# Performance work log

Measured on AMD Instinct MI355X. Metric: run time of the kernel, lower is better.

The kernel has to match this reference:

```python
import jax, jax.numpy as jnp
import numpy as np

B, T, V, F = 32, 128, 128, 64
K_ORDER = 3
N_FILT = 64

def setup_inputs() -> dict:
    key = jax.random.key(0)
    k1, k2, k3 = jax.random.split(key, 3)
    x = jax.random.normal(k1, (B, T, V, F), dtype=jnp.float32)
    W = jax.random.uniform(k2, (B, V, V), dtype=jnp.float32)  # learned adjacency, nonneg
    # keras 'uniform' initializer default range [-0.05, 0.05]
    Theta = jax.random.uniform(k3, (K_ORDER, F, N_FILT), dtype=jnp.float32, minval=-0.05, maxval=0.05)
    return {"x": x, "W": W, "Theta": Theta}

def reference(x, W, Theta):
    # x: (B,T,V,F), W: (B,V,V), Theta: (k,F,O)
    k = Theta.shape[0]
    v = x.shape[2]
    eye = jnp.eye(v, dtype=x.dtype)
    deg = jnp.sum(W, axis=1)                      # (B,V) -- sum over axis=1 as in K.sum(W, axis=1)
    D = eye[None, :, :] * deg[:, :, None]         # matrix_diag(deg)
    L = D - W
    L_t = L - eye[None, :, :]                     # 2*L/lambda_max - I with lambda_max=2
    chebs = [jnp.broadcast_to(eye[None, :, :], W.shape), L_t]
    for i in range(2, k):
        # NOTE: elementwise multiply, faithful to the original tf code (tf `*`)
        chebs.append(2.0 * L_t * chebs[-1] - chebs[-2])
    Tk = jnp.stack(chebs, axis=0)                 # (k,B,V,V)
    # out[b,t,u,o] = sum_{k,v,f} Tk[k,b,v,u] * x[b,t,v,f] * Theta[k,f,o]
    # (T_k transposed matmul graph_signal, then dot with theta_k, summed over k and t-batched)
    out = jnp.einsum('kbvu,btvf,kfo->btuo', Tk, x, Theta)
    return jax.nn.relu(out)
```

## Files before the change

### kernel.cpp

```cpp
#include <hip/hip_runtime.h>

typedef __attribute__((ext_vector_type(8))) short bf16x8;
typedef __attribute__((ext_vector_type(4))) float f32x4;

namespace {

constexpr int B = 32, T = 128, V = 128, F = 64, O = 64;
constexpr int TPB = 8;

constexpr size_t WS_THT_OFF = (size_t)B * 64 * 64 * 8 * 2;
constexpr size_t WS_LDG_OFF = WS_THT_OFF + 1536 * 8 * 2;

__device__ inline unsigned short f2bf(float f) {
    unsigned u = __builtin_bit_cast(unsigned, f);
    u += 0x7FFFu + ((u >> 16) & 1u);
    return (unsigned short)(u >> 16);
}

__global__ __launch_bounds__(256) void prep(const float* __restrict__ W,
                                            const float* __restrict__ Theta,
                                            unsigned short* __restrict__ acat_f,
                                            unsigned short* __restrict__ tht_f,
                                            float* __restrict__ ldg) {
    const int tid = threadIdx.x;
    if (blockIdx.x == B) {
        for (int i = 0; i < 6; ++i) {
            int fi = tid + i * 256;
            int ks = fi / 768, rem = fi % 768;
            int nf = rem >> 6, lane = rem & 63;
            int n = nf * 16 + (lane & 15);
            int f0 = ks * 32 + (lane >> 4) * 8;
            unsigned short vals[8];
#pragma unroll
            for (int j = 0; j < 8; ++j) {
                int f = f0 + j;
                float v;
                if (n < 64)       v = Theta[f * 64 + n] - Theta[2 * 4096 + f * 64 + n];
                else if (n < 128) v = Theta[4096 + f * 64 + (n - 64)];
                else              v = Theta[2 * 4096 + f * 64 + (n - 128)];
                vals[j] = f2bf(v);
            }
            *(bf16x8*)(tht_f + (size_t)fi * 8) = *(bf16x8*)vals;
        }
        return;
    }
    const int b = blockIdx.x;
    const float* Wb = W + (size_t)b * V * V;
    __shared__ float Wl[V][V + 1];
    for (int i = 0; i < V * V / 256; ++i) {
        int idx = tid + i * 256;
        Wl[idx >> 7][idx & 127] = Wb[idx];
    }
    __syncthreads();
    if (tid < V) {
        float s = 0.f;
        for (int i = 0; i < V; ++i) s += Wl[i][tid];
        ldg[b * V + tid] = s - 1.0f - Wl[tid][tid];
    }
    unsigned short* ab_f = acat_f + (size_t)b * 32768;
    for (int i = 0; i < 16; ++i) {
        int fi = tid + i * 256;
        int ks = fi >> 9, rem = fi & 511;
        int r2 = rem >> 6, lane = rem & 63;
        int u = r2 * 16 + (lane & 15);
        int kv0 = ks * 32 + (lane >> 4) * 8;
        unsigned short vals[8];
#pragma unroll
        for (int j = 0; j < 8; ++j) {
            int kv = kv0 + j, v = kv & 127;
            float wv = Wl[v][u];
            float val = (v == u) ? 0.f : ((kv < 128) ? -wv : 2.f * wv * wv);
            vals[j] = f2bf(val);
        }
        *(bf16x8*)(ab_f + (size_t)fi * 8) = *(bf16x8*)vals;
    }
}

__global__ __launch_bounds__(512, 4) void graph_conv_main(
    const float* __restrict__ x, const unsigned short* __restrict__ acat_f,
    const unsigned short* __restrict__ tht_f, const float* __restrict__ ldg,
    float* __restrict__ out) {
    const int t0 = blockIdx.x * TPB, b = blockIdx.y;
    const int tid = threadIdx.x;
    const int lane = tid & 63, w = tid >> 6;
    const int lr = lane & 15, lg = lane >> 4;

    __shared__ __align__(16) unsigned short tht_s[12288];
    __shared__ __align__(16) unsigned short xbuf[2][8192];
    __shared__ __align__(16) unsigned short zc1[4096];
    __shared__ __align__(16) unsigned short zc2[4096];

    const float* xb = x + ((size_t)(b * T + t0)) * (V * F);

#pragma unroll
    for (int i = 0; i < 3; ++i) {
        int c = tid + i * 512;
        __builtin_amdgcn_global_load_lds(
            (const __attribute__((address_space(1))) void*)(tht_f + c * 8),
            (__attribute__((address_space(3))) void*)(tht_s + c * 8), 16, 0, 0);
    }

    bf16x8 af_r[8];
#pragma unroll
    for (int ks = 0; ks < 8; ++ks)
        af_r[ks] = *(const bf16x8*)(acat_f + (((size_t)b * 64 + ks * 8 + w) * 64 + lane) * 8);

    const float* ldb = ldg + b * V;
    const f32x4 ldv = *(const f32x4*)(ldb + 16 * w + lg * 4);
    const f32x4 ld2v = 2.0f * ldv * ldv;

    float4 pf[4];
    auto load_pf = [&](int tt) {
        const float4* src = (const float4*)(xb + (size_t)tt * (V * F));
#pragma unroll
        for (int i = 0; i < 4; ++i) pf[i] = src[tid + i * 512];
    };
    auto store_pf = [&](int buf) {
#pragma unroll
        for (int i = 0; i < 4; ++i) {
            int p = tid + i * 512;
            int row = p >> 4, c4 = p & 15;
            uint2 q;
            q.x = f2bf(pf[i].x) | ((unsigned)f2bf(pf[i].y) << 16);
            q.y = f2bf(pf[i].z) | ((unsigned)f2bf(pf[i].w) << 16);
            *(uint2*)((char*)xbuf[buf] + row * 128 + ((c4 * 8) ^ ((row & 7) << 4))) = q;
        }
    };

    load_pf(0);
    store_pf(0);
    __syncthreads();
    int cur = 0;

    for (int tt = 0; tt < TPB; ++tt) {
        if (tt + 1 < TPB) load_pf(tt + 1);

        bf16x8 xa[2];
        {
            const int row = 16 * w + lr;
            const int rb = row * 128, rs = (row & 7) << 4;
#pragma unroll
            for (int ks = 0; ks < 2; ++ks)
                xa[ks] = *(const bf16x8*)((const char*)xbuf[cur] + rb + ((ks * 64 + lg * 16) ^ rs));
        }

        f32x4 acc[4], z[4];
#pragma unroll
        for (int of = 0; of < 4; ++of) {
            acc[of] = (f32x4){0.f, 0.f, 0.f, 0.f};
            z[of] = (f32x4){0.f, 0.f, 0.f, 0.f};
        }

#pragma unroll
        for (int ks = 0; ks < 2; ++ks)
#pragma unroll
            for (int nf = 0; nf < 8; ++nf) {
                bf16x8 tb = *(const bf16x8*)(tht_s + ((ks * 12 + nf) * 64 + lane) * 8);
                if (nf < 4) acc[nf] = __builtin_amdgcn_mfma_f32_16x16x32_bf16(xa[ks], tb, acc[nf], 0, 0, 0);
                else        z[nf - 4] = __builtin_amdgcn_mfma_f32_16x16x32_bf16(xa[ks], tb, z[nf - 4], 0, 0, 0);
            }

        {
            const int vcol = 16 * w + lg * 4;
#pragma unroll
            for (int of = 0; of < 4; ++of) {
                acc[of] += ldv * z[of];
                const int rowz = of * 16 + lr;
                f32x4 zv = z[of];
                uint2 q;
                q.x = f2bf(zv[0]) | ((unsigned)f2bf(zv[1]) << 16);
                q.y = f2bf(zv[2]) | ((unsigned)f2bf(zv[3]) << 16);
                *(uint2*)((char*)zc1 + rowz * 256 + ((vcol * 2) ^ ((rowz & 7) << 4))) = q;
                z[of] = (f32x4){0.f, 0.f, 0.f, 0.f};
            }
        }

#pragma unroll
        for (int ks = 0; ks < 2; ++ks)
#pragma unroll
            for (int nf = 0; nf < 4; ++nf) {
                bf16x8 tb = *(const bf16x8*)(tht_s + ((ks * 12 + 8 + nf) * 64 + lane) * 8);
                z[nf] = __builtin_amdgcn_mfma_f32_16x16x32_bf16(xa[ks], tb, z[nf], 0, 0, 0);
            }

        {
            const int vcol = 16 * w + lg * 4;
#pragma unroll
            for (int of = 0; of < 4; ++of) {
                acc[of] += ld2v * z[of];
                const int rowz = of * 16 + lr;
                f32x4 zv = z[of];
                uint2 q;
                q.x = f2bf(zv[0]) | ((unsigned)f2bf(zv[1]) << 16);
                q.y = f2bf(zv[2]) | ((unsigned)f2bf(zv[3]) << 16);
                *(uint2*)((char*)zc2 + rowz * 256 + ((vcol * 2) ^ ((rowz & 7) << 4))) = q;
            }
        }

        __syncthreads();

#pragma unroll
        for (int ks = 0; ks < 8; ++ks) {
            const char* zsrc = (ks < 4) ? (const char*)zc1 : (const char*)zc2;
            const int kcol = (ks & 3) * 64 + lg * 16;
#pragma unroll
            for (int of = 0; of < 4; ++of) {
                const int rowz = of * 16 + lr;
                bf16x8 zb = *(const bf16x8*)(zsrc + rowz * 256 + (kcol ^ ((rowz & 7) << 4)));
                acc[of] = __builtin_amdgcn_mfma_f32_16x16x32_bf16(af_r[ks], zb, acc[of], 0, 0, 0);
            }
        }

        if (tt + 1 < TPB) store_pf(cur ^ 1);

        float* obt = out + ((size_t)(b * T + t0 + tt)) * (V * O);
#pragma unroll
        for (int of = 0; of < 4; ++of)
#pragma unroll
            for (int j = 0; j < 4; ++j) {
                const int u = 16 * w + lg * 4 + j;
                const int o = of * 16 + lr;
                const float r = acc[of][j];
                obt[u * 64 + o] = r > 0.f ? r : 0.f;
            }

        __syncthreads();
        cur ^= 1;
    }
}

}

extern "C" void kernel_launch(void* const* d_in, const int* in_sizes, int n_in,
                              void* d_out, int out_size, void* d_ws, size_t ws_size,
                              hipStream_t stream) {
    const float* x = (const float*)d_in[0];
    const float* W = (const float*)d_in[1];
    const float* Theta = (const float*)d_in[2];
    float* outp = (float*)d_out;

    unsigned short* acat_f = (unsigned short*)d_ws;
    unsigned short* tht_f = (unsigned short*)((char*)d_ws + WS_THT_OFF);
    float* ldg = (float*)((char*)d_ws + WS_LDG_OFF);

    prep<<<B + 1, 256, 0, stream>>>(W, Theta, acat_f, tht_f, ldg);
    graph_conv_main<<<dim3(T / TPB, B), 512, 0, stream>>>(x, acat_f, tht_f, ldg, outp);
}
```

Baseline: 85.19 us.

## Stage x via async global-to-LDS loads in fp32 and double time steps per block

```diff
diff --git a/kernel.cpp b/kernel.cpp
--- a/kernel.cpp
+++ b/kernel.cpp
@@ -6,7 +6,7 @@
 namespace {
 
 constexpr int B = 32, T = 128, V = 128, F = 64, O = 64;
-constexpr int TPB = 8;
+constexpr int TPB = 16;
 
 constexpr size_t WS_THT_OFF = (size_t)B * 64 * 64 * 8 * 2;
 constexpr size_t WS_LDG_OFF = WS_THT_OFF + 1536 * 8 * 2;
@@ -76,7 +76,7 @@
     }
 }
 
-__global__ __launch_bounds__(512, 4) void graph_conv_main(
+__global__ __launch_bounds__(512, 2) void graph_conv_main(
     const float* __restrict__ x, const unsigned short* __restrict__ acat_f,
     const unsigned short* __restrict__ tht_f, const float* __restrict__ ldg,
     float* __restrict__ out) {
@@ -86,11 +86,37 @@
     const int lr = lane & 15, lg = lane >> 4;
 
     __shared__ __align__(16) unsigned short tht_s[12288];
-    __shared__ __align__(16) unsigned short xbuf[2][8192];
-    __shared__ __align__(16) unsigned short zc1[4096];
-    __shared__ __align__(16) unsigned short zc2[4096];
+    __shared__ __align__(16) float xbuf[2][V * F];
+    __shared__ __align__(16) unsigned short zc1[8192];
+    __shared__ __align__(16) unsigned short zc2[8192];
 
     const float* xb = x + ((size_t)(b * T + t0)) * (V * F);
+
+    bf16x8 af_r[8];
+#pragma unroll
+    for (int ks = 0; ks < 8; ++ks)
+        af_r[ks] = *(const bf16x8*)(acat_f + (((size_t)b * 64 + ks * 8 + w) * 64 + lane) * 8);
+    const f32x4 ldv = *(const f32x4*)(ldg + b * V + 16 * w + lg * 4);
+    const f32x4 ld2v = 2.0f * ldv * ldv;
+    asm volatile("s_waitcnt vmcnt(0)" ::: "memory");
+    __builtin_amdgcn_sched_barrier(0);
+
+    auto stage_x = [&](int tt, int buf) {
+        const char* src = (const char*)(xb + (size_t)tt * (V * F));
+        char* lbase = (char*)&xbuf[buf][0] + w * 4096;
+#pragma unroll
+        for (int j = 0; j < 4; ++j) {
+            int a = j * 1024 + lane * 16;
+            int rloc = a >> 8;
+            int slot = (a >> 5) & 7;
+            int within = a & 31;
+            int row = 16 * w + rloc;
+            const char* g = src + row * 256 + ((slot ^ (row & 7)) << 5) + within;
+            __builtin_amdgcn_global_load_lds(
+                (const __attribute__((address_space(1))) void*)g,
+                (__attribute__((address_space(3))) void*)(lbase + j * 1024), 16, 0, 0);
+        }
+    };
 
 #pragma unroll
     for (int i = 0; i < 3; ++i) {
@@ -99,49 +125,35 @@
             (const __attribute__((address_space(1))) void*)(tht_f + c * 8),
             (__attribute__((address_space(3))) void*)(tht_s + c * 8), 16, 0, 0);
     }
-
-    bf16x8 af_r[8];
-#pragma unroll
-    for (int ks = 0; ks < 8; ++ks)
-        af_r[ks] = *(const bf16x8*)(acat_f + (((size_t)b * 64 + ks * 8 + w) * 64 + lane) * 8);
-
-    const float* ldb = ldg + b * V;
-    const f32x4 ldv = *(const f32x4*)(ldb + 16 * w + lg * 4);
-    const f32x4 ld2v = 2.0f * ldv * ldv;
-
-    float4 pf[4];
-    auto load_pf = [&](int tt) {
-        const float4* src = (const float4*)(xb + (size_t)tt * (V * F));
-#pragma unroll
-        for (int i = 0; i < 4; ++i) pf[i] = src[tid + i * 512];
-    };
-    auto store_pf = [&](int buf) {
-#pragma unroll
-        for (int i = 0; i < 4; ++i) {
-            int p = tid + i * 512;
-            int row = p >> 4, c4 = p & 15;
-            uint2 q;
-            q.x = f2bf(pf[i].x) | ((unsigned)f2bf(pf[i].y) << 16);
-            q.y = f2bf(pf[i].z) | ((unsigned)f2bf(pf[i].w) << 16);
-            *(uint2*)((char*)xbuf[buf] + row * 128 + ((c4 * 8) ^ ((row & 7) << 4))) = q;
-        }
-    };
-
-    load_pf(0);
-    store_pf(0);
-    __syncthreads();
+    stage_x(0, 0);
+    asm volatile("s_waitcnt vmcnt(0)" ::: "memory");
+    __builtin_amdgcn_sched_barrier(0);
+    __builtin_amdgcn_s_barrier();
+    __builtin_amdgcn_sched_barrier(0);
+
     int cur = 0;
-
     for (int tt = 0; tt < TPB; ++tt) {
-        if (tt + 1 < TPB) load_pf(tt + 1);
+        if (tt + 1 < TPB) stage_x(tt + 1, cur ^ 1);
+        asm volatile("s_waitcnt vmcnt(4)" ::: "memory");
+        __builtin_amdgcn_sched_barrier(0);
 
         bf16x8 xa[2];
         {
             const int row = 16 * w + lr;
-            const int rb = row * 128, rs = (row & 7) << 4;
-#pragma unroll
-            for (int ks = 0; ks < 2; ++ks)
-                xa[ks] = *(const bf16x8*)((const char*)xbuf[cur] + rb + ((ks * 64 + lg * 16) ^ rs));
+            const char* rbp = (const char*)&xbuf[cur][0] + row * 256;
+            const int rs = row & 7;
+#pragma unroll
+            for (int ks = 0; ks < 2; ++ks) {
+                const char* pa = rbp + (((ks * 4 + lg) ^ rs) << 5);
+                f32x4 a0 = *(const f32x4*)pa;
+                f32x4 a1 = *(const f32x4*)(pa + 16);
+                uint4 u;
+                u.x = f2bf(a0[0]) | ((unsigned)f2bf(a0[1]) << 16);
+                u.y = f2bf(a0[2]) | ((unsigned)f2bf(a0[3]) << 16);
+                u.z = f2bf(a1[0]) | ((unsigned)f2bf(a1[1]) << 16);
+                u.w = f2bf(a1[2]) | ((unsigned)f2bf(a1[3]) << 16);
+                xa[ks] = __builtin_bit_cast(bf16x8, u);
+            }
         }
 
         f32x4 acc[4], z[4];
@@ -197,7 +209,10 @@
             }
         }
 
-        __syncthreads();
+        asm volatile("s_waitcnt lgkmcnt(0)" ::: "memory");
+        __builtin_amdgcn_sched_barrier(0);
+        __builtin_amdgcn_s_barrier();
+        __builtin_amdgcn_sched_barrier(0);
 
 #pragma unroll
         for (int ks = 0; ks < 8; ++ks) {
@@ -210,8 +225,6 @@
                 acc[of] = __builtin_amdgcn_mfma_f32_16x16x32_bf16(af_r[ks], zb, acc[of], 0, 0, 0);
             }
         }
-
-        if (tt + 1 < TPB) store_pf(cur ^ 1);
 
         float* obt = out + ((size_t)(b * T + t0 + tt)) * (V * O);
 #pragma unroll
@@ -224,7 +237,10 @@
                 obt[u * 64 + o] = r > 0.f ? r : 0.f;
             }
 
-        __syncthreads();
+        asm volatile("s_waitcnt lgkmcnt(0)" ::: "memory");
+        __builtin_amdgcn_sched_barrier(0);
+        __builtin_amdgcn_s_barrier();
+        __builtin_amdgcn_sched_barrier(0);
         cur ^= 1;
     }
 }
```

After: 87.94 us. 3.2% more time.
